# Kernel tuning notes

Hardware: AMD Instinct MI355X
Metric: run time of the kernel (lower is better)

The kernel has to match this reference:

```python
import jax, jax.numpy as jnp
import numpy as np

D = 2048   # dec_hidden_size == enc_hidden_size
IN = 512   # input_size
T = 4096   # T_enc


def setup_inputs() -> dict:
    key = jax.random.key(0)
    ks = jax.random.split(key, 20)
    s = 0.02
    zeros = jnp.zeros
    return {
        "data": jax.random.normal(ks[0], (1, IN), jnp.float32),
        "h0": jax.random.normal(ks[1], (1, 1, D), jnp.float32),
        "c0": jax.random.normal(ks[2], (1, 1, D), jnp.float32),
        "enc_output": jax.random.normal(ks[3], (T, 1, D), jnp.float32),
        "pi": jax.random.normal(ks[4], (T,), jnp.float32),
        "W_w": jax.random.normal(ks[5], (D, D), jnp.float32) * s,
        "U_w": jax.random.normal(ks[6], (D, D), jnp.float32) * s,
        "V_w": jax.random.normal(ks[7], (1, D), jnp.float32) * s,
        "lin_w": jax.random.normal(ks[8], (D, D), jnp.float32) * s,
        "lin_b": zeros((D,), jnp.float32),
        "lin1_w": jax.random.normal(ks[9], (D, D), jnp.float32) * s,
        "lin1_b": zeros((D,), jnp.float32),
        "lin2_w": jax.random.normal(ks[10], (D, D), jnp.float32) * s,
        "lin2_b": zeros((D,), jnp.float32),
        "dense_w": jax.random.normal(ks[11], (1, D), jnp.float32) * s,
        "dense_b": zeros((1,), jnp.float32),
        "W_ih": jax.random.normal(ks[12], (4 * D, IN + D), jnp.float32) * s,
        "W_hh": jax.random.normal(ks[13], (4 * D, D), jnp.float32) * s,
        "b_ih": zeros((4 * D,), jnp.float32),
        "b_hh": zeros((4 * D,), jnp.float32),
        "i": 100,
    }


def reference(data, h0, c0, enc_output, pi, W_w, U_w, V_w, lin_w, lin_b,
              lin1_w, lin1_b, lin2_w, lin2_b, dense_w, dense_b,
              W_ih, W_hh, b_ih, b_hh, i):
    Tl = pi.shape[0]
    output_pos = i + 1
    enc = enc_output[:, 0, :]                      # (T, E)
    # binary_vector(output_pos, T) @ pi : row k gets pi[output_pos+T-k-2] iff k >= output_pos-1
    k = jnp.arange(Tl)
    idx = output_pos + Tl - k - 2
    prod = jnp.where(k >= output_pos - 1, pi[jnp.clip(idx, 0, Tl - 1)], 0.0)
    u_h = (enc @ U_w.T) * prod[:, None]            # (T, D), per-channel scale by prod
    q = h0[0, 0] @ W_w.T                           # (D,)
    score = jnp.tanh(q[None, :] + u_h) @ V_w[0]    # (T,)
    score = jnp.where(k < output_pos, 0.0, score)  # attn_score[:j_null] = 0 (zero, not -inf)
    attn = jax.nn.softmax(score)                   # softmax over T
    context = attn @ enc                           # (E,)
    x = jnp.concatenate([context, data[0]])        # (E + IN,)
    # single-step LSTM, PyTorch gate order i,f,g,o
    gates = x @ W_ih.T + b_ih + h0[0, 0] @ W_hh.T + b_hh
    gi, gf, gg, go = jnp.split(gates, 4)
    c_new = jax.nn.sigmoid(gf) * c0[0, 0] + jax.nn.sigmoid(gi) * jnp.tanh(gg)
    h_new = jax.nn.sigmoid(go) * jnp.tanh(c_new)
    fc = h_new @ lin_w.T + lin_b
    l1 = fc @ lin1_w.T + lin1_b
    delta = jax.nn.softmax(l1)
    beta = jax.nn.softplus(fc @ lin2_w.T + lin2_b)
    gamma = l1 @ dense_w.T + dense_b               # original reuses linear1 for lin3
    return (gamma, beta, delta, h_new, c_new)
```

## Files before the change

### kernel.cpp

```cpp
#include <hip/hip_runtime.h>
#include <hip/hip_bf16.h>

#define D_  2048
#define IN_ 512
#define T_  4096
#define G4_ 8192

typedef __attribute__((ext_vector_type(4))) float f32x4;
typedef __attribute__((ext_vector_type(8))) short s16x8;
typedef unsigned short u16;

#define WS_PROD    0
#define WS_Q       (T_)
#define WS_X       (T_ + D_)
#define WS_PARTIAL (WS_X + D_ + IN_)
#define WS_ATTN    (WS_PARTIAL + T_*16)
#define WS_GATES   (WS_ATTN + T_)
#define WS_G2      (WS_GATES + G4_)
#define WS_FC      (WS_G2 + G4_)
#define WS_L1      (WS_FC + D_)
#define WS_HN      (WS_L1 + D_)
#define WS_BF16    (WS_HN + D_)
#define WS_FAST_BYTES ((size_t)WS_BF16 * 4 + ((size_t)T_ * D_ + (size_t)D_ * D_) * 2)

typedef const __attribute__((address_space(1))) void gas_t;
typedef __attribute__((address_space(3))) void las_t;

__device__ inline u16 bfbits(float f) {
  union { __hip_bfloat16 b; u16 s; } u; u.b = __float2bfloat16(f); return u.s;
}
__device__ inline float bf2f(u16 s) {
  union { unsigned u; float f; } v; v.u = ((unsigned)s) << 16; return v.f;
}

__device__ inline float wave_dot4(const float* __restrict__ w,
                                  const float* __restrict__ x, int n4, int lane) {
  float s = 0.f;
  const f32x4* w4 = (const f32x4*)w;
  const f32x4* x4 = (const f32x4*)x;
  for (int c = lane; c < n4; c += 64) {
    f32x4 a = w4[c], b = x4[c];
    s += a[0]*b[0] + a[1]*b[1] + a[2]*b[2] + a[3]*b[3];
  }
  #pragma unroll
  for (int m = 32; m >= 1; m >>= 1) s += __shfl_xor(s, m, 64);
  return s;
}

__global__ __launch_bounds__(256) void k_prep(const float* __restrict__ Ww,
    const float* __restrict__ h0, const float* __restrict__ pi,
    const float* __restrict__ data, const int* __restrict__ ip,
    const float* __restrict__ enc, const float* __restrict__ Uw,
    int do_convert, float* __restrict__ ws) {
  const int tid = threadIdx.x, bid = blockIdx.x;
  const int gidx = bid * 256 + tid;
  const int op = ip[0] + 1;
  if (gidx < T_) {
    float p = 0.f;
    if (gidx >= op - 1) {
      int idx = op + T_ - gidx - 2;
      idx = idx < 0 ? 0 : (idx > T_ - 1 ? T_ - 1 : idx);
      p = pi[idx];
    }
    ws[WS_PROD + gidx] = p;
  }
  if (gidx < D_) ws[WS_X + gidx] = 0.f;
  if (gidx < IN_) ws[WS_X + D_ + gidx] = data[gidx];
  const int wid = tid >> 6, lane = tid & 63;
  const int row = bid * 4 + wid;
  if (row < D_) {
    float s = wave_dot4(Ww + (size_t)row * D_, h0, D_ / 4, lane);
    if (lane == 0) ws[WS_Q + row] = s;
  }
  if (do_convert) {
    u16* encB = (u16*)(ws + WS_BF16);
    u16* UwB  = encB + (size_t)T_ * D_;
    const size_t nth = 512u * 256u;
    for (size_t base = (size_t)gidx * 8; base < (size_t)T_ * D_; base += nth * 8) {
      f32x4 v0 = *(const f32x4*)(enc + base);
      f32x4 v1 = *(const f32x4*)(enc + base + 4);
      u16 t[8];
      #pragma unroll
      for (int e = 0; e < 4; ++e) { t[e] = bfbits(v0[e]); t[4 + e] = bfbits(v1[e]); }
      *(s16x8*)&encB[base] = *(s16x8*)&t[0];
    }
    for (size_t base = (size_t)gidx * 8; base < (size_t)D_ * D_; base += nth * 8) {
      f32x4 v0 = *(const f32x4*)(Uw + base);
      f32x4 v1 = *(const f32x4*)(Uw + base + 4);
      u16 t[8];
      #pragma unroll
      for (int e = 0; e < 4; ++e) { t[e] = bfbits(v0[e]); t[4 + e] = bfbits(v1[e]); }
      *(s16x8*)&UwB[base] = *(s16x8*)&t[0];
    }
  }
}

__global__ __launch_bounds__(512, 4) void k_gemm_bf16(
    const float* __restrict__ Vw, const float* __restrict__ h0,
    const float* __restrict__ Whh, float* __restrict__ ws) {
  __shared__ __align__(16) u16 Ah[128 * 64];
  __shared__ __align__(16) u16 Bh[128 * 64];
  const u16* encB = (const u16*)(ws + WS_BF16);
  const u16* UwB  = encB + (size_t)T_ * D_;
  const int tid = threadIdx.x, lane = tid & 63, wid = tid >> 6;
  const int wr = wid >> 2, wc = wid & 3;
  const int g = lane >> 4, lr = lane & 15;
  const int bid = blockIdx.x;
  const int wgid = (bid & 7) * 64 + (bid >> 3);
  const int mb = wgid >> 4, nb = wgid & 15;

  f32x4 acc[4][2];
  #pragma unroll
  for (int m = 0; m < 4; ++m)
    #pragma unroll
    for (int n = 0; n < 2; ++n) acc[m][n] = (f32x4){0.f, 0.f, 0.f, 0.f};

  const int c0 = tid,        r0 = c0 >> 3, s0 = (c0 & 7) ^ (r0 & 7);
  const int c1 = tid + 512,  r1 = c1 >> 3, s1 = (c1 & 7) ^ (r1 & 7);
  const u16* ga0 = encB + (size_t)(mb * 128 + r0) * D_ + s0 * 8;
  const u16* ga1 = encB + (size_t)(mb * 128 + r1) * D_ + s1 * 8;
  const u16* gb0 = UwB  + (size_t)(nb * 128 + r0) * D_ + s0 * 8;
  const u16* gb1 = UwB  + (size_t)(nb * 128 + r1) * D_ + s1 * 8;
  u16* la0 = &Ah[c0 * 8]; u16* la1 = &Ah[c1 * 8];
  u16* lb0 = &Bh[c0 * 8]; u16* lb1 = &Bh[c1 * 8];

  for (int ks = 0; ks < D_ / 64; ++ks) {
    __syncthreads();
    __builtin_amdgcn_global_load_lds((gas_t*)(ga0 + ks * 64), (las_t*)la0, 16, 0, 0);
    __builtin_amdgcn_global_load_lds((gas_t*)(ga1 + ks * 64), (las_t*)la1, 16, 0, 0);
    __builtin_amdgcn_global_load_lds((gas_t*)(gb0 + ks * 64), (las_t*)lb0, 16, 0, 0);
    __builtin_amdgcn_global_load_lds((gas_t*)(gb1 + ks * 64), (las_t*)lb1, 16, 0, 0);
    __syncthreads();
    #pragma unroll
    for (int kk = 0; kk < 2; ++kk) {
      const int koff = kk * 64 + g * 16;
      s16x8 af[4], bf[2];
      #pragma unroll
      for (int m = 0; m < 4; ++m) {
        const int r = wr * 64 + m * 16 + lr;
        af[m] = *(const s16x8*)((const char*)Ah + r * 128 + (koff ^ ((r & 7) << 4)));
      }
      #pragma unroll
      for (int n = 0; n < 2; ++n) {
        const int r = wc * 32 + n * 16 + lr;
        bf[n] = *(const s16x8*)((const char*)Bh + r * 128 + (koff ^ ((r & 7) << 4)));
      }
      #pragma unroll
      for (int m = 0; m < 4; ++m)
        #pragma unroll
        for (int n = 0; n < 2; ++n)
          acc[m][n] = __builtin_amdgcn_mfma_f32_16x16x32_bf16(af[m], bf[n], acc[m][n], 0, 0, 0);
    }
  }

  const float* q    = ws + WS_Q;
  const float* prod = ws + WS_PROD;
  float Vv[2], qv[2];
  #pragma unroll
  for (int n = 0; n < 2; ++n) {
    const int d = nb * 128 + wc * 32 + n * 16 + lr;
    Vv[n] = Vw[d]; qv[n] = q[d];
  }
  __syncthreads();
  float* red = (float*)Ah;
  #pragma unroll
  for (int m = 0; m < 4; ++m) {
    #pragma unroll
    for (int r = 0; r < 4; ++r) {
      const int t_loc = wr * 64 + m * 16 + g * 4 + r;
      const float p = prod[mb * 128 + t_loc];
      float s = Vv[0] * tanhf(qv[0] + p * acc[m][0][r])
              + Vv[1] * tanhf(qv[1] + p * acc[m][1][r]);
      s += __shfl_xor(s, 1, 64);
      s += __shfl_xor(s, 2, 64);
      s += __shfl_xor(s, 4, 64);
      s += __shfl_xor(s, 8, 64);
      if (lr == 0) red[t_loc * 4 + wc] = s;
    }
  }
  __syncthreads();
  if (tid < 128) {
    const float s = red[tid * 4] + red[tid * 4 + 1] + red[tid * 4 + 2] + red[tid * 4 + 3];
    ws[WS_PARTIAL + (size_t)(mb * 128 + tid) * 16 + nb] = s;
  }

  const int rbase = bid * 16 + wid * 2;
  #pragma unroll
  for (int rr = 0; rr < 2; ++rr) {
    const int row = rbase + rr;
    float s = wave_dot4(Whh + (size_t)row * D_, h0, D_ / 4, lane);
    if (lane == 0) ws[WS_G2 + row] = s;
  }
}

__global__ __launch_bounds__(512, 4) void k_gemm_f32(
    const float* __restrict__ enc, const float* __restrict__ Uw,
    const float* __restrict__ Vw, const float* __restrict__ h0,
    const float* __restrict__ Whh, float* __restrict__ ws) {
  __shared__ __align__(16) u16 sbuf[2 * 128 * 40];
  u16* Ah = sbuf;
  u16* Bh = sbuf + 128 * 40;
  const int tid = threadIdx.x;
  const int lane = tid & 63, wid = tid >> 6;
  const int wr = wid >> 2, wc = wid & 3;
  const int g = lane >> 4, lr = lane & 15;
  const int mb = blockIdx.x, nb = blockIdx.y;

  f32x4 acc[4][2];
  #pragma unroll
  for (int m = 0; m < 4; ++m)
    #pragma unroll
    for (int n = 0; n < 2; ++n) acc[m][n] = (f32x4){0.f, 0.f, 0.f, 0.f};

  const int srow = tid >> 2;
  const int scol = (tid & 3) * 8;
  const float* pa0 = enc + (size_t)(mb * 128 + srow) * D_ + scol;
  const float* pb0 = Uw  + (size_t)(nb * 128 + srow) * D_ + scol;
  const int sidx = srow * 40 + scol;

  f32x4 an0 = *(const f32x4*)(pa0);
  f32x4 an1 = *(const f32x4*)(pa0 + 4);
  f32x4 bn0 = *(const f32x4*)(pb0);
  f32x4 bn1 = *(const f32x4*)(pb0 + 4);

  for (int ks = 0; ks < 64; ++ks) {
    f32x4 a0 = an0, a1 = an1, b0 = bn0, b1 = bn1;
    if (ks < 63) {
      an0 = *(const f32x4*)(pa0 + (ks + 1) * 32);
      an1 = *(const f32x4*)(pa0 + (ks + 1) * 32 + 4);
      bn0 = *(const f32x4*)(pb0 + (ks + 1) * 32);
      bn1 = *(const f32x4*)(pb0 + (ks + 1) * 32 + 4);
    }
    __syncthreads();
    __align__(16) u16 ah[8], bh[8];
    #pragma unroll
    for (int e = 0; e < 4; ++e) {
      ah[e] = bfbits(a0[e]); ah[4 + e] = bfbits(a1[e]);
      bh[e] = bfbits(b0[e]); bh[4 + e] = bfbits(b1[e]);
    }
    *(s16x8*)&Ah[sidx] = *(s16x8*)&ah[0];
    *(s16x8*)&Bh[sidx] = *(s16x8*)&bh[0];
    __syncthreads();

    s16x8 af[4], bf[2];
    #pragma unroll
    for (int m = 0; m < 4; ++m)
      af[m] = *(const s16x8*)&Ah[(wr * 64 + m * 16 + lr) * 40 + g * 8];
    #pragma unroll
    for (int n = 0; n < 2; ++n)
      bf[n] = *(const s16x8*)&Bh[(wc * 32 + n * 16 + lr) * 40 + g * 8];
    #pragma unroll
    for (int m = 0; m < 4; ++m)
      #pragma unroll
      for (int n = 0; n < 2; ++n)
        acc[m][n] = __builtin_amdgcn_mfma_f32_16x16x32_bf16(af[m], bf[n], acc[m][n], 0, 0, 0);
  }

  const float* q    = ws + WS_Q;
  const float* prod = ws + WS_PROD;
  float Vv[2], qv[2];
  #pragma unroll
  for (int n = 0; n < 2; ++n) {
    const int d = nb * 128 + wc * 32 + n * 16 + lr;
    Vv[n] = Vw[d]; qv[n] = q[d];
  }
  __syncthreads();
  float* red = (float*)sbuf;
  #pragma unroll
  for (int m = 0; m < 4; ++m) {
    #pragma unroll
    for (int r = 0; r < 4; ++r) {
      const int t_loc = wr * 64 + m * 16 + g * 4 + r;
      const float p = prod[mb * 128 + t_loc];
      float s = Vv[0] * tanhf(qv[0] + p * acc[m][0][r])
              + Vv[1] * tanhf(qv[1] + p * acc[m][1][r]);
      s += __shfl_xor(s, 1, 64);
      s += __shfl_xor(s, 2, 64);
      s += __shfl_xor(s, 4, 64);
      s += __shfl_xor(s, 8, 64);
      if (lr == 0) red[t_loc * 4 + wc] = s;
    }
  }
  __syncthreads();
  if (tid < 128) {
    const float s = red[tid * 4] + red[tid * 4 + 1] + red[tid * 4 + 2] + red[tid * 4 + 3];
    ws[WS_PARTIAL + (size_t)(mb * 128 + tid) * 16 + nb] = s;
  }
  const int flat = blockIdx.y * gridDim.x + blockIdx.x;
  const int rbase = flat * 16 + wid * 2;
  #pragma unroll
  for (int rr = 0; rr < 2; ++rr) {
    const int row = rbase + rr;
    float s = wave_dot4(Whh + (size_t)row * D_, h0, D_ / 4, lane);
    if (lane == 0) ws[WS_G2 + row] = s;
  }
}

__global__ __launch_bounds__(1024) void k_attn(const int* __restrict__ ip,
                                               float* __restrict__ ws) {
  __shared__ float sm[16];
  const int tid = threadIdx.x, lane = tid & 63, wid = tid >> 6;
  const int op = ip[0] + 1;
  float v[4];
  #pragma unroll
  for (int j = 0; j < 4; ++j) {
    const int t = tid + j * 1024;
    const float* p = ws + WS_PARTIAL + (size_t)t * 16;
    float s = 0.f;
    #pragma unroll
    for (int c = 0; c < 16; ++c) s += p[c];
    v[j] = (t < op) ? 0.f : s;
  }
  float mx = fmaxf(fmaxf(v[0], v[1]), fmaxf(v[2], v[3]));
  #pragma unroll
  for (int m = 32; m >= 1; m >>= 1) mx = fmaxf(mx, __shfl_xor(mx, m, 64));
  if (lane == 0) sm[wid] = mx;
  __syncthreads();
  if (tid == 0) {
    float m2 = sm[0];
    for (int w = 1; w < 16; ++w) m2 = fmaxf(m2, sm[w]);
    sm[0] = m2;
  }
  __syncthreads();
  mx = sm[0];
  __syncthreads();
  float e[4], ls = 0.f;
  #pragma unroll
  for (int j = 0; j < 4; ++j) { e[j] = expf(v[j] - mx); ls += e[j]; }
  #pragma unroll
  for (int m = 32; m >= 1; m >>= 1) ls += __shfl_xor(ls, m, 64);
  if (lane == 0) sm[wid] = ls;
  __syncthreads();
  if (tid == 0) {
    float s2 = 0.f;
    for (int w = 0; w < 16; ++w) s2 += sm[w];
    sm[0] = s2;
  }
  __syncthreads();
  const float inv = 1.f / sm[0];
  #pragma unroll
  for (int j = 0; j < 4; ++j) ws[WS_ATTN + tid + j * 1024] = e[j] * inv;
}

__global__ __launch_bounds__(256) void k_context_bf16(float* __restrict__ ws) {
  const u16* encB = (const u16*)(ws + WS_BF16);
  const int d = blockIdx.x * 256 + threadIdx.x;
  const int t0 = blockIdx.y * 256;
  const float* attn = ws + WS_ATTN;
  float s = 0.f;
  for (int t = t0; t < t0 + 256; ++t) s += attn[t] * bf2f(encB[(size_t)t * D_ + d]);
  atomicAdd(&ws[WS_X + d], s);
}
__global__ __launch_bounds__(256) void k_context_f32(const float* __restrict__ enc,
                                                     float* __restrict__ ws) {
  const int d = blockIdx.x * 256 + threadIdx.x;
  const int t0 = blockIdx.y * 256;
  const float* attn = ws + WS_ATTN;
  float s = 0.f;
  for (int t = t0; t < t0 + 256; ++t) s += attn[t] * enc[(size_t)t * D_ + d];
  atomicAdd(&ws[WS_X + d], s);
}

__global__ __launch_bounds__(256) void k_gates(const float* __restrict__ Wih,
    const float* __restrict__ bih, const float* __restrict__ bhh,
    float* __restrict__ ws) {
  const int wid = threadIdx.x >> 6, lane = threadIdx.x & 63;
  const int row = blockIdx.x * 4 + wid;
  float s = wave_dot4(Wih + (size_t)row * (D_ + IN_), ws + WS_X, (D_ + IN_) / 4, lane);
  if (lane == 0) ws[WS_GATES + row] = s + ws[WS_G2 + row] + bih[row] + bhh[row];
}

__global__ __launch_bounds__(256) void k_cell(const float* __restrict__ c0,
    float* __restrict__ ws, float* __restrict__ out) {
  const int d = blockIdx.x * 256 + threadIdx.x;
  const float* gt = ws + WS_GATES;
  const float gi = gt[d], gf = gt[D_ + d], gg = gt[2 * D_ + d], go = gt[3 * D_ + d];
  const float si = 1.f / (1.f + expf(-gi));
  const float sf = 1.f / (1.f + expf(-gf));
  const float so = 1.f / (1.f + expf(-go));
  const float cn = sf * c0[d] + si * tanhf(gg);
  const float hn = so * tanhf(cn);
  out[1 + 2 * D_ + d] = hn;
  out[1 + 3 * D_ + d] = cn;
  ws[WS_HN + d] = hn;
}

__global__ __launch_bounds__(256) void k_fc(const float* __restrict__ lw,
    const float* __restrict__ lb, float* __restrict__ ws) {
  const int wid = threadIdx.x >> 6, lane = threadIdx.x & 63;
  const int row = blockIdx.x * 4 + wid;
  float s = wave_dot4(lw + (size_t)row * D_, ws + WS_HN, D_ / 4, lane);
  if (lane == 0) ws[WS_FC + row] = s + lb[row];
}

__global__ __launch_bounds__(256) void k_l1beta(const float* __restrict__ l1w,
    const float* __restrict__ l1b, const float* __restrict__ l2w,
    const float* __restrict__ l2b, float* __restrict__ ws, float* __restrict__ out) {
  const int wid = threadIdx.x >> 6, lane = threadIdx.x & 63;
  const int row = blockIdx.x * 4 + wid;
  float a = wave_dot4(l1w + (size_t)row * D_, ws + WS_FC, D_ / 4, lane);
  float b = wave_dot4(l2w + (size_t)row * D_, ws + WS_FC, D_ / 4, lane);
  if (lane == 0) {
    ws[WS_L1 + row] = a + l1b[row];
    const float x = b + l2b[row];
    out[1 + row] = (x > 20.f) ? x : log1pf(expf(x));
  }
}

__global__ __launch_bounds__(256) void k_final(const float* __restrict__ dw,
    const float* __restrict__ db, float* __restrict__ ws, float* __restrict__ out) {
  __shared__ float sm[4];
  const int tid = threadIdx.x, lane = tid & 63, wid = tid >> 6;
  float v[8];
  #pragma unroll
  for (int j = 0; j < 8; ++j) v[j] = ws[WS_L1 + tid + j * 256];
  float mx = v[0];
  #pragma unroll
  for (int j = 1; j < 8; ++j) mx = fmaxf(mx, v[j]);
  #pragma unroll
  for (int m = 32; m >= 1; m >>= 1) mx = fmaxf(mx, __shfl_xor(mx, m, 64));
  if (lane == 0) sm[wid] = mx;
  __syncthreads();
  mx = fmaxf(fmaxf(sm[0], sm[1]), fmaxf(sm[2], sm[3]));
  __syncthreads();
  float e[8], ls = 0.f;
  #pragma unroll
  for (int j = 0; j < 8; ++j) { e[j] = expf(v[j] - mx); ls += e[j]; }
  #pragma unroll
  for (int m = 32; m >= 1; m >>= 1) ls += __shfl_xor(ls, m, 64);
  if (lane == 0) sm[wid] = ls;
  __syncthreads();
  ls = sm[0] + sm[1] + sm[2] + sm[3];
  __syncthreads();
  const float inv = 1.f / ls;
  float gp = 0.f;
  #pragma unroll
  for (int j = 0; j < 8; ++j) {
    out[1 + D_ + tid + j * 256] = e[j] * inv;
    gp += v[j] * dw[tid + j * 256];
  }
  #pragma unroll
  for (int m = 32; m >= 1; m >>= 1) gp += __shfl_xor(gp, m, 64);
  if (lane == 0) sm[wid] = gp;
  __syncthreads();
  if (tid == 0) out[0] = sm[0] + sm[1] + sm[2] + sm[3] + db[0];
}

extern "C" void kernel_launch(void* const* d_in, const int* in_sizes, int n_in,
                              void* d_out, int out_size, void* d_ws, size_t ws_size,
                              hipStream_t stream) {
  (void)in_sizes; (void)n_in; (void)out_size;
  const float* data   = (const float*)d_in[0];
  const float* h0     = (const float*)d_in[1];
  const float* c0     = (const float*)d_in[2];
  const float* enc    = (const float*)d_in[3];
  const float* pi     = (const float*)d_in[4];
  const float* Ww     = (const float*)d_in[5];
  const float* Uw     = (const float*)d_in[6];
  const float* Vw     = (const float*)d_in[7];
  const float* lin_w  = (const float*)d_in[8];
  const float* lin_b  = (const float*)d_in[9];
  const float* lin1_w = (const float*)d_in[10];
  const float* lin1_b = (const float*)d_in[11];
  const float* lin2_w = (const float*)d_in[12];
  const float* lin2_b = (const float*)d_in[13];
  const float* dw     = (const float*)d_in[14];
  const float* db     = (const float*)d_in[15];
  const float* Wih    = (const float*)d_in[16];
  const float* Whh    = (const float*)d_in[17];
  const float* bih    = (const float*)d_in[18];
  const float* bhh    = (const float*)d_in[19];
  const int*   ip     = (const int*)d_in[20];
  float* ws  = (float*)d_ws;
  float* out = (float*)d_out;
  const int fast = (ws_size >= WS_FAST_BYTES) ? 1 : 0;

  k_prep<<<512, 256, 0, stream>>>(Ww, h0, pi, data, ip, enc, Uw, fast, ws);
  if (fast)
    k_gemm_bf16<<<512, 512, 0, stream>>>(Vw, h0, Whh, ws);
  else
    k_gemm_f32<<<dim3(T_ / 128, D_ / 128), 512, 0, stream>>>(enc, Uw, Vw, h0, Whh, ws);
  k_attn<<<1, 1024, 0, stream>>>(ip, ws);
  if (fast)
    k_context_bf16<<<dim3(D_ / 256, T_ / 256), 256, 0, stream>>>(ws);
  else
    k_context_f32<<<dim3(D_ / 256, T_ / 256), 256, 0, stream>>>(enc, ws);
  k_gates<<<G4_ / 4, 256, 0, stream>>>(Wih, bih, bhh, ws);
  k_cell<<<D_ / 256, 256, 0, stream>>>(c0, ws, out);
  k_fc<<<D_ / 4, 256, 0, stream>>>(lin_w, lin_b, ws);
  k_l1beta<<<D_ / 4, 256, 0, stream>>>(lin1_w, lin1_b, lin2_w, lin2_b, ws, out);
  k_final<<<1, 256, 0, stream>>>(dw, db, ws, out);
}
```

Measured before the change: 137.0 us.

## Double-buffer bf16 GEMM LDS tiles and widen conversion prep kernel

```diff
diff --git a/kernel.cpp b/kernel.cpp
--- a/kernel.cpp
+++ b/kernel.cpp
@@ -47,13 +47,35 @@
   return s;
 }
 
-__global__ __launch_bounds__(256) void k_prep(const float* __restrict__ Ww,
+__global__ __launch_bounds__(256) void k_convert(const float* __restrict__ Ww,
     const float* __restrict__ h0, const float* __restrict__ pi,
     const float* __restrict__ data, const int* __restrict__ ip,
     const float* __restrict__ enc, const float* __restrict__ Uw,
     int do_convert, float* __restrict__ ws) {
-  const int tid = threadIdx.x, bid = blockIdx.x;
-  const int gidx = bid * 256 + tid;
+  const int gidx = blockIdx.x * 256 + threadIdx.x;
+  const int nth = 1024 * 256;
+  if (do_convert) {
+    u16* encB = (u16*)(ws + WS_BF16);
+    u16* UwB  = encB + (size_t)T_ * D_;
+    for (int c = gidx; c < (T_ * D_) / 8; c += nth) {
+      const size_t base = (size_t)c * 8;
+      f32x4 v0 = *(const f32x4*)(enc + base);
+      f32x4 v1 = *(const f32x4*)(enc + base + 4);
+      u16 t[8];
+      #pragma unroll
+      for (int e = 0; e < 4; ++e) { t[e] = bfbits(v0[e]); t[4 + e] = bfbits(v1[e]); }
+      *(s16x8*)&encB[base] = *(s16x8*)&t[0];
+    }
+    for (int c = gidx; c < (D_ * D_) / 8; c += nth) {
+      const size_t base = (size_t)c * 8;
+      f32x4 v0 = *(const f32x4*)(Uw + base);
+      f32x4 v1 = *(const f32x4*)(Uw + base + 4);
+      u16 t[8];
+      #pragma unroll
+      for (int e = 0; e < 4; ++e) { t[e] = bfbits(v0[e]); t[4 + e] = bfbits(v1[e]); }
+      *(s16x8*)&UwB[base] = *(s16x8*)&t[0];
+    }
+  }
   const int op = ip[0] + 1;
   if (gidx < T_) {
     float p = 0.f;
@@ -66,40 +88,18 @@
   }
   if (gidx < D_) ws[WS_X + gidx] = 0.f;
   if (gidx < IN_) ws[WS_X + D_ + gidx] = data[gidx];
-  const int wid = tid >> 6, lane = tid & 63;
-  const int row = bid * 4 + wid;
-  if (row < D_) {
-    float s = wave_dot4(Ww + (size_t)row * D_, h0, D_ / 4, lane);
-    if (lane == 0) ws[WS_Q + row] = s;
-  }
-  if (do_convert) {
-    u16* encB = (u16*)(ws + WS_BF16);
-    u16* UwB  = encB + (size_t)T_ * D_;
-    const size_t nth = 512u * 256u;
-    for (size_t base = (size_t)gidx * 8; base < (size_t)T_ * D_; base += nth * 8) {
-      f32x4 v0 = *(const f32x4*)(enc + base);
-      f32x4 v1 = *(const f32x4*)(enc + base + 4);
-      u16 t[8];
-      #pragma unroll
-      for (int e = 0; e < 4; ++e) { t[e] = bfbits(v0[e]); t[4 + e] = bfbits(v1[e]); }
-      *(s16x8*)&encB[base] = *(s16x8*)&t[0];
-    }
-    for (size_t base = (size_t)gidx * 8; base < (size_t)D_ * D_; base += nth * 8) {
-      f32x4 v0 = *(const f32x4*)(Uw + base);
-      f32x4 v1 = *(const f32x4*)(Uw + base + 4);
-      u16 t[8];
-      #pragma unroll
-      for (int e = 0; e < 4; ++e) { t[e] = bfbits(v0[e]); t[4 + e] = bfbits(v1[e]); }
-      *(s16x8*)&UwB[base] = *(s16x8*)&t[0];
-    }
+  const int gw = gidx >> 6, lane = gidx & 63;
+  if (gw < D_) {
+    float s = wave_dot4(Ww + (size_t)gw * D_, h0, D_ / 4, lane);
+    if (lane == 0) ws[WS_Q + gw] = s;
   }
 }
 
 __global__ __launch_bounds__(512, 4) void k_gemm_bf16(
     const float* __restrict__ Vw, const float* __restrict__ h0,
     const float* __restrict__ Whh, float* __restrict__ ws) {
-  __shared__ __align__(16) u16 Ah[128 * 64];
-  __shared__ __align__(16) u16 Bh[128 * 64];
+  __shared__ __align__(16) u16 Ah[2][128 * 64];
+  __shared__ __align__(16) u16 Bh[2][128 * 64];
   const u16* encB = (const u16*)(ws + WS_BF16);
   const u16* UwB  = encB + (size_t)T_ * D_;
   const int tid = threadIdx.x, lane = tid & 63, wid = tid >> 6;
@@ -121,16 +121,24 @@
   const u16* ga1 = encB + (size_t)(mb * 128 + r1) * D_ + s1 * 8;
   const u16* gb0 = UwB  + (size_t)(nb * 128 + r0) * D_ + s0 * 8;
   const u16* gb1 = UwB  + (size_t)(nb * 128 + r1) * D_ + s1 * 8;
-  u16* la0 = &Ah[c0 * 8]; u16* la1 = &Ah[c1 * 8];
-  u16* lb0 = &Bh[c0 * 8]; u16* lb1 = &Bh[c1 * 8];
-
-  for (int ks = 0; ks < D_ / 64; ++ks) {
-    __syncthreads();
-    __builtin_amdgcn_global_load_lds((gas_t*)(ga0 + ks * 64), (las_t*)la0, 16, 0, 0);
-    __builtin_amdgcn_global_load_lds((gas_t*)(ga1 + ks * 64), (las_t*)la1, 16, 0, 0);
-    __builtin_amdgcn_global_load_lds((gas_t*)(gb0 + ks * 64), (las_t*)lb0, 16, 0, 0);
-    __builtin_amdgcn_global_load_lds((gas_t*)(gb1 + ks * 64), (las_t*)lb1, 16, 0, 0);
-    __syncthreads();
+
+  #define STAGE_(kt, b) do { \
+    __builtin_amdgcn_global_load_lds((gas_t*)(ga0 + (kt) * 64), (las_t*)&Ah[b][c0 * 8], 16, 0, 0); \
+    __builtin_amdgcn_global_load_lds((gas_t*)(ga1 + (kt) * 64), (las_t*)&Ah[b][c1 * 8], 16, 0, 0); \
+    __builtin_amdgcn_global_load_lds((gas_t*)(gb0 + (kt) * 64), (las_t*)&Bh[b][c0 * 8], 16, 0, 0); \
+    __builtin_amdgcn_global_load_lds((gas_t*)(gb1 + (kt) * 64), (las_t*)&Bh[b][c1 * 8], 16, 0, 0); \
+  } while (0)
+
+  STAGE_(0, 0);
+
+  for (int ks = 0; ks < 32; ++ks) {
+    const int cur = ks & 1;
+    if (ks < 31) STAGE_(ks + 1, cur ^ 1);
+    __builtin_amdgcn_sched_barrier(0);
+    if (ks < 31) asm volatile("s_waitcnt vmcnt(4)" ::: "memory");
+    else         asm volatile("s_waitcnt vmcnt(0)" ::: "memory");
+    __builtin_amdgcn_sched_barrier(0);
+    __builtin_amdgcn_s_barrier();
     #pragma unroll
     for (int kk = 0; kk < 2; ++kk) {
       const int koff = kk * 64 + g * 16;
@@ -138,12 +146,12 @@
       #pragma unroll
       for (int m = 0; m < 4; ++m) {
         const int r = wr * 64 + m * 16 + lr;
-        af[m] = *(const s16x8*)((const char*)Ah + r * 128 + (koff ^ ((r & 7) << 4)));
+        af[m] = *(const s16x8*)((const char*)&Ah[cur][0] + r * 128 + (koff ^ ((r & 7) << 4)));
       }
       #pragma unroll
       for (int n = 0; n < 2; ++n) {
         const int r = wc * 32 + n * 16 + lr;
-        bf[n] = *(const s16x8*)((const char*)Bh + r * 128 + (koff ^ ((r & 7) << 4)));
+        bf[n] = *(const s16x8*)((const char*)&Bh[cur][0] + r * 128 + (koff ^ ((r & 7) << 4)));
       }
       #pragma unroll
       for (int m = 0; m < 4; ++m)
@@ -151,7 +159,12 @@
         for (int n = 0; n < 2; ++n)
           acc[m][n] = __builtin_amdgcn_mfma_f32_16x16x32_bf16(af[m], bf[n], acc[m][n], 0, 0, 0);
     }
-  }
+    __builtin_amdgcn_sched_barrier(0);
+    asm volatile("s_waitcnt lgkmcnt(0)" ::: "memory");
+    __builtin_amdgcn_sched_barrier(0);
+    __builtin_amdgcn_s_barrier();
+  }
+  #undef STAGE_
 
   const float* q    = ws + WS_Q;
   const float* prod = ws + WS_PROD;
@@ -162,7 +175,7 @@
     Vv[n] = Vw[d]; qv[n] = q[d];
   }
   __syncthreads();
-  float* red = (float*)Ah;
+  float* red = (float*)&Ah[0][0];
   #pragma unroll
   for (int m = 0; m < 4; ++m) {
     #pragma unroll
@@ -305,10 +318,10 @@
   #pragma unroll
   for (int j = 0; j < 4; ++j) {
     const int t = tid + j * 1024;
-    const float* p = ws + WS_PARTIAL + (size_t)t * 16;
-    float s = 0.f;
-    #pragma unroll
-    for (int c = 0; c < 16; ++c) s += p[c];
+    const f32x4* p = (const f32x4*)(ws + WS_PARTIAL + (size_t)t * 16);
+    f32x4 p0 = p[0], p1 = p[1], p2 = p[2], p3 = p[3];
+    float s = (p0[0]+p0[1]+p0[2]+p0[3]) + (p1[0]+p1[1]+p1[2]+p1[3])
+            + (p2[0]+p2[1]+p2[2]+p2[3]) + (p3[0]+p3[1]+p3[2]+p3[3]);
     v[j] = (t < op) ? 0.f : s;
   }
   float mx = fmaxf(fmaxf(v[0], v[1]), fmaxf(v[2], v[3]));
@@ -475,7 +488,7 @@
   float* out = (float*)d_out;
   const int fast = (ws_size >= WS_FAST_BYTES) ? 1 : 0;
 
-  k_prep<<<512, 256, 0, stream>>>(Ww, h0, pi, data, ip, enc, Uw, fast, ws);
+  k_convert<<<1024, 256, 0, stream>>>(Ww, h0, pi, data, ip, enc, Uw, fast, ws);
   if (fast)
     k_gemm_bf16<<<512, 512, 0, stream>>>(Vw, h0, Whh, ws);
   else
```

After: 135.2 us. Within noise of the previous version (-1.3%).
